# Optimization experiments

Hardware: AMD Instinct MI355X
Metric: run time of the kernel (lower is better)

Reference implementation:

```python
import jax, jax.numpy as jnp
import numpy as np

B, L, E, D, H, N_ENT = 64, 50, 50, 100, 100, 200000


def setup_inputs() -> dict:
    key = jax.random.key(0)
    ks = jax.random.split(key, 12)
    neighbor_ids = jax.random.randint(ks[0], (B, L, E), 0, N_ENT)
    # 0/1 adjacency; mimic GraphConstructer: symmetric with self-loops
    adj = jax.random.randint(ks[1], (B, L, E, E), 0, 2).astype(jnp.int32)
    adj = jnp.maximum(adj, adj.transpose(0, 1, 3, 2))
    adj = jnp.maximum(adj, jnp.eye(E, dtype=jnp.int32))
    s = 0.1  # ~ 1/sqrt(D) init scale
    emb = jax.random.normal(ks[2], (N_ENT, D), jnp.float32) * s
    Wq = jax.random.normal(ks[3], (D, H), jnp.float32) * s
    bq = jax.random.normal(ks[4], (H,), jnp.float32) * s
    Wk = jax.random.normal(ks[5], (D, H), jnp.float32) * s
    bk = jax.random.normal(ks[6], (H,), jnp.float32) * s
    Wv = jax.random.normal(ks[7], (D, H), jnp.float32) * s
    bv = jax.random.normal(ks[8], (H,), jnp.float32) * s
    Ws = jax.random.normal(ks[9], (D, H), jnp.float32) * s
    bs = jax.random.normal(ks[10], (H,), jnp.float32) * s
    return {"neighbor_ids": neighbor_ids, "adj": adj, "emb": emb,
            "Wq": Wq, "bq": bq, "Wk": Wk, "bk": bk,
            "Wv": Wv, "bv": bv, "Ws": Ws, "bs": bs}


def reference(neighbor_ids, adj, emb, Wq, bq, Wk, bk, Wv, bv, Ws, bs):
    b, l, e = neighbor_ids.shape
    d = emb.shape[1]
    h = Wq.shape[1]
    # embedding gather: [B,L,E,D] -> [G,E,D], G = B*L graphs
    x = emb[neighbor_ids].reshape(b * l, e, d)
    a = adj.reshape(b * l, e, e)
    # TransformerConv (heads=1): q,k,v linear with bias
    q = x @ Wq + bq
    k = x @ Wk + bk
    v = x @ Wv + bv
    scores = jnp.einsum('gid,gjd->gij', q, k) / jnp.sqrt(jnp.asarray(h, x.dtype))
    # edge (j -> i) exists when adj[j, i] != 0; target i attends over sources j
    mask = a.transpose(0, 2, 1) != 0  # mask[g, i, j]
    neg = jnp.finfo(scores.dtype).min
    attn = jax.nn.softmax(jnp.where(mask, scores, neg), axis=-1)
    # nodes with no incoming edge aggregate to zero (PyG softmax/scatter semantics)
    attn = jnp.where(mask.any(-1, keepdims=True), attn, jnp.zeros((), attn.dtype))
    agg = jnp.einsum('gij,gjd->gid', attn, v)
    out = agg + x @ Ws + bs  # root/skip connection with bias
    # take center node (index 0) of each ego-graph -> [B, L, H]
    return out.reshape(b, l, e, h)[:, :, 0, :]
```

## Files before the change

kernel.cpp:

```cpp
#include <hip/hip_runtime.h>
#include <math.h>

#define E_N 50
#define D_N 100
#define H_N 100
#define XSTR 51
#define GT 8
#define NTHR 256
#define GATHER_IT 5

__device__ __forceinline__ float bf2f(unsigned int s16) {
    return __uint_as_float(s16 << 16);
}

__device__ __forceinline__ unsigned short f2bf(float f) {
    unsigned int u = __float_as_uint(f);
    unsigned int r = (u + 0x7FFFu + ((u >> 16) & 1u)) >> 16;
    return (unsigned short)r;
}

template <bool F32>
__device__ __forceinline__ float ldx(const void* p, int i) {
    if (F32) return reinterpret_cast<const float*>(p)[i];
    return bf2f(reinterpret_cast<const unsigned short*>(p)[i]);
}

template <bool F32>
__device__ __forceinline__ float4 ld4(const void* p, long long i4) {
    if (F32) return reinterpret_cast<const float4*>(p)[i4];
    uint2 v = reinterpret_cast<const uint2*>(p)[i4];
    float4 f;
    f.x = bf2f(v.x & 0xFFFFu);
    f.y = bf2f(v.x >> 16);
    f.z = bf2f(v.y & 0xFFFFu);
    f.w = bf2f(v.y >> 16);
    return f;
}

__device__ __forceinline__ int sniff_f32(const void* emb, int tid, int* slot) {
    if (tid < 64) {
        unsigned short hw = reinterpret_cast<const unsigned short*>(emb)[tid * 2];
        float v = bf2f(hw);
        float a = fabsf(v);
        int sane = (v == 0.f) || (a >= 1e-4f && a <= 8.0f);
        unsigned long long ball = __ballot(sane);
        if (tid == 0) *slot = (__popcll(ball) < 32) ? 1 : 0;
    }
    __syncthreads();
    return *slot;
}

template <bool F32>
__device__ __forceinline__ void precomp_core(
    int dp, int tid, const void* __restrict__ Wq, const void* __restrict__ bq,
    const void* __restrict__ Wk, float* __restrict__ At, float* __restrict__ c,
    float* wq_s, float* bq_s)
{
    if (tid < H_N) wq_s[tid] = ldx<F32>(Wq, dp * H_N + tid);
    if (dp == 0 && tid < H_N) bq_s[tid] = ldx<F32>(bq, tid);
    __syncthreads();
    if (tid < D_N) {
        float a0 = 0.f, a1 = 0.f, a2 = 0.f, a3 = 0.f;
        #pragma unroll
        for (int h4 = 0; h4 < H_N / 4; ++h4) {
            float4 w = ld4<F32>(Wk, (long long)tid * (H_N / 4) + h4);
            a0 = fmaf(w.x, wq_s[h4 * 4 + 0], a0);
            a1 = fmaf(w.y, wq_s[h4 * 4 + 1], a1);
            a2 = fmaf(w.z, wq_s[h4 * 4 + 2], a2);
            a3 = fmaf(w.w, wq_s[h4 * 4 + 3], a3);
        }
        At[dp * D_N + tid] = (a0 + a1) + (a2 + a3);
        if (dp == 0) {
            float c0 = 0.f, c1 = 0.f, c2 = 0.f, c3 = 0.f;
            #pragma unroll
            for (int h4 = 0; h4 < H_N / 4; ++h4) {
                float4 w = ld4<F32>(Wk, (long long)tid * (H_N / 4) + h4);
                c0 = fmaf(w.x, bq_s[h4 * 4 + 0], c0);
                c1 = fmaf(w.y, bq_s[h4 * 4 + 1], c1);
                c2 = fmaf(w.z, bq_s[h4 * 4 + 2], c2);
                c3 = fmaf(w.w, bq_s[h4 * 4 + 3], c3);
            }
            c[tid] = (c0 + c1) + (c2 + c3);
        }
    }
}

__global__ __launch_bounds__(128)
void precomp_kernel(const void* __restrict__ Wq, const void* __restrict__ bq,
                    const void* __restrict__ Wk, const void* __restrict__ emb,
                    float* __restrict__ At, float* __restrict__ c)
{
    __shared__ float wq_s[H_N];
    __shared__ float bq_s[H_N];
    __shared__ int is_f32_s;
    int f32 = sniff_f32(emb, threadIdx.x, &is_f32_s);
    if (f32) precomp_core<true >(blockIdx.x, threadIdx.x, Wq, bq, Wk, At, c, wq_s, bq_s);
    else     precomp_core<false>(blockIdx.x, threadIdx.x, Wq, bq, Wk, At, c, wq_s, bq_s);
}

template <bool F32>
__device__ __forceinline__ void ka_core(
    int g0, int G, int tid,
    const int* __restrict__ nbr, const void* __restrict__ emb,
    const float* __restrict__ At, const float* __restrict__ c,
    const void* __restrict__ Ws,
    float* __restrict__ wl, float* __restrict__ skip, float* x0s)
{
    if (tid < GT * (D_N / 4)) {
        int q = tid / (D_N / 4), d4 = tid - q * (D_N / 4);
        int gq = g0 + q; if (gq >= G) gq = G - 1;
        int id0 = nbr[gq * E_N];
        float4 v = ld4<F32>(emb, (long long)id0 * (D_N / 4) + d4);
        reinterpret_cast<float4*>(x0s + q * D_N)[d4] = v;
    }
    __syncthreads();

    if (tid < D_N) {
        int d = tid;
        float cv = c[d];
        float acc[GT];
        #pragma unroll
        for (int q = 0; q < GT; ++q) acc[q] = cv;
        #pragma unroll 4
        for (int dp = 0; dp < D_N; ++dp) {
            float a = At[dp * D_N + d];
            #pragma unroll
            for (int q = 0; q < GT; ++q)
                acc[q] = fmaf(a, x0s[q * D_N + dp], acc[q]);
        }
        #pragma unroll
        for (int q = 0; q < GT; ++q) {
            int gq = g0 + q;
            if (gq < G) wl[(size_t)gq * D_N + d] = acc[q];
        }
    } else if (tid >= 128 && tid < 128 + H_N) {
        int h = tid - 128;
        float acc[GT];
        #pragma unroll
        for (int q = 0; q < GT; ++q) acc[q] = 0.f;
        #pragma unroll 4
        for (int d = 0; d < D_N; ++d) {
            float w = ldx<F32>(Ws, d * H_N + h);
            #pragma unroll
            for (int q = 0; q < GT; ++q)
                acc[q] = fmaf(w, x0s[q * D_N + d], acc[q]);
        }
        #pragma unroll
        for (int q = 0; q < GT; ++q) {
            int gq = g0 + q;
            if (gq < G) skip[(size_t)gq * H_N + h] = acc[q];
        }
    }
}

__global__ __launch_bounds__(NTHR)
void ka_kernel(const int* __restrict__ nbr, const void* __restrict__ emb,
               const float* __restrict__ At, const float* __restrict__ c,
               const void* __restrict__ Ws,
               float* __restrict__ wl, float* __restrict__ skip, int G)
{
    __shared__ __align__(16) float x0s[GT * D_N];
    __shared__ int is_f32_s;
    int f32 = sniff_f32(emb, threadIdx.x, &is_f32_s);
    if (f32) ka_core<true >(blockIdx.x * GT, G, threadIdx.x, nbr, emb, At, c, Ws, wl, skip, x0s);
    else     ka_core<false>(blockIdx.x * GT, G, threadIdx.x, nbr, emb, At, c, Ws, wl, skip, x0s);
}

template <bool F32>
__device__ __forceinline__ void kb_core(
    int g, int tid,
    const int* __restrict__ nbr, const int* __restrict__ adj,
    const void* __restrict__ emb,
    const float* __restrict__ wl, float* __restrict__ y, float* __restrict__ den,
    float* xs, float* wls, float* ps)
{
    float wlv = (tid < D_N) ? wl[(size_t)g * D_N + tid] : 0.f;
    int mk = (tid < E_N) ? adj[(size_t)g * (E_N * E_N) + tid * E_N] : 0;
    int idr[GATHER_IT];
    #pragma unroll
    for (int r = 0; r < GATHER_IT; ++r) {
        int i = tid + NTHR * r;
        idr[r] = (i < E_N * (D_N / 4)) ? nbr[g * E_N + i / 25] : 0;
    }
    if (tid < D_N) wls[tid] = wlv;

    #pragma unroll
    for (int r = 0; r < GATHER_IT; ++r) {
        int i = tid + NTHR * r;
        if (i < E_N * (D_N / 4)) {
            int j  = i / 25;
            int d4 = i - j * 25;
            float4 v = ld4<F32>(emb, (long long)idr[r] * (D_N / 4) + d4);
            int d0 = d4 * 4;
            xs[(d0 + 0) * XSTR + j] = v.x;
            xs[(d0 + 1) * XSTR + j] = v.y;
            xs[(d0 + 2) * XSTR + j] = v.z;
            xs[(d0 + 3) * XSTR + j] = v.w;
        }
    }
    __syncthreads();

    if (tid < 64) {
        float s = 0.f;
        if (tid < E_N) {
            #pragma unroll 10
            for (int d = 0; d < D_N; ++d)
                s = fmaf(wls[d], xs[d * XSTR + tid], s);
            s *= 0.1f;
        }
        bool live = (tid < E_N) && (mk != 0);
        float m = live ? s : -3.0e38f;
        #pragma unroll
        for (int off = 32; off; off >>= 1)
            m = fmaxf(m, __shfl_xor(m, off));
        float e = live ? __expf(s - m) : 0.f;
        float dn = e;
        #pragma unroll
        for (int off = 32; off; off >>= 1)
            dn += __shfl_xor(dn, off);
        float inv = dn > 0.f ? 1.0f / dn : 0.f;
        if (tid < E_N) ps[tid] = e * inv;
        if (tid == 0)  den[g] = dn;
    }
    __syncthreads();

    if (tid < D_N) {
        float acc = 0.f;
        #pragma unroll 10
        for (int j = 0; j < E_N; ++j)
            acc = fmaf(ps[j], xs[tid * XSTR + j], acc);
        y[(size_t)g * D_N + tid] = acc;
    }
}

__global__ __launch_bounds__(NTHR)
void kb_kernel(const int* __restrict__ nbr, const int* __restrict__ adj,
               const void* __restrict__ emb,
               const float* __restrict__ wl, float* __restrict__ y,
               float* __restrict__ den, int G)
{
    __shared__ __align__(16) float xs[D_N * XSTR];
    __shared__ __align__(16) float wls[D_N];
    __shared__ __align__(16) float ps[E_N];
    __shared__ int is_f32_s;
    int f32 = sniff_f32(emb, threadIdx.x, &is_f32_s);
    if (f32) kb_core<true >(blockIdx.x, threadIdx.x, nbr, adj, emb, wl, y, den, xs, wls, ps);
    else     kb_core<false>(blockIdx.x, threadIdx.x, nbr, adj, emb, wl, y, den, xs, wls, ps);
}

template <bool F32>
__device__ __forceinline__ void kc_core(
    int g0, int G, int tid,
    const void* __restrict__ Wv, const void* __restrict__ bv,
    const void* __restrict__ bs,
    const float* __restrict__ skip, const float* __restrict__ y,
    const float* __restrict__ den, void* __restrict__ out,
    float* ys, float* denf)
{
    if (tid < GT * (D_N / 4)) {
        int q = tid / (D_N / 4), d4 = tid - q * (D_N / 4);
        int gq = g0 + q; if (gq >= G) gq = G - 1;
        reinterpret_cast<float4*>(ys + q * D_N)[d4] =
            reinterpret_cast<const float4*>(y + (size_t)gq * D_N)[d4];
    }
    if (tid < GT) {
        int gq = g0 + tid; if (gq >= G) gq = G - 1;
        denf[tid] = den[gq];
    }
    __syncthreads();

    int half = tid >> 7;
    int hh = tid & 127;
    if (hh < H_N) {
        int h = hh, qb = half * 4;
        float b   = ldx<F32>(bs, h);
        float bvv = ldx<F32>(bv, h);
        float acc[4];
        #pragma unroll
        for (int q2 = 0; q2 < 4; ++q2) {
            int gq = g0 + qb + q2; if (gq >= G) gq = G - 1;
            acc[q2] = b + (denf[qb + q2] > 0.f ? bvv : 0.f) + skip[(size_t)gq * H_N + h];
        }
        #pragma unroll 4
        for (int d = 0; d < D_N; ++d) {
            float w = ldx<F32>(Wv, d * H_N + h);
            #pragma unroll
            for (int q2 = 0; q2 < 4; ++q2)
                acc[q2] = fmaf(w, ys[(qb + q2) * D_N + d], acc[q2]);
        }
        #pragma unroll
        for (int q2 = 0; q2 < 4; ++q2) {
            int gq = g0 + qb + q2;
            if (gq < G) {
                size_t o = (size_t)gq * H_N + h;
                if (F32) reinterpret_cast<float*>(out)[o] = acc[q2];
                else     reinterpret_cast<unsigned short*>(out)[o] = f2bf(acc[q2]);
            }
        }
    }
}

__global__ __launch_bounds__(NTHR)
void kc_kernel(const void* __restrict__ Wv, const void* __restrict__ bv,
               const void* __restrict__ bs, const void* __restrict__ emb,
               const float* __restrict__ skip, const float* __restrict__ y,
               const float* __restrict__ den, void* __restrict__ out, int G)
{
    __shared__ __align__(16) float ys[GT * D_N];
    __shared__ float denf[GT];
    __shared__ int is_f32_s;
    int f32 = sniff_f32(emb, threadIdx.x, &is_f32_s);
    if (f32) kc_core<true >(blockIdx.x * GT, G, threadIdx.x, Wv, bv, bs, skip, y, den, out, ys, denf);
    else     kc_core<false>(blockIdx.x * GT, G, threadIdx.x, Wv, bv, bs, skip, y, den, out, ys, denf);
}

extern "C" void kernel_launch(void* const* d_in, const int* in_sizes, int n_in,
                              void* d_out, int out_size, void* d_ws, size_t ws_size,
                              hipStream_t stream) {
    const int* nbr = (const int*)d_in[0];
    const int* adj = (const int*)d_in[1];
    const void* emb = d_in[2];
    const void* Wq  = d_in[3];
    const void* bq  = d_in[4];
    const void* Wk  = d_in[5];
    const void* Wv  = d_in[7];
    const void* bv  = d_in[8];
    const void* Ws  = d_in[9];
    const void* bs  = d_in[10];

    const int G = in_sizes[0] / E_N;

    float* At   = (float*)d_ws;
    float* c    = At + D_N * D_N;
    float* wl   = c + D_N;
    float* skip = wl + (size_t)G * D_N;
    float* y    = skip + (size_t)G * H_N;
    float* den  = y + (size_t)G * D_N;

    const int GB = (G + GT - 1) / GT;
    precomp_kernel<<<D_N, 128, 0, stream>>>(Wq, bq, Wk, emb, At, c);
    ka_kernel<<<GB, NTHR, 0, stream>>>(nbr, emb, At, c, Ws, wl, skip, G);
    kb_kernel<<<G, NTHR, 0, stream>>>(nbr, adj, emb, wl, y, den, G);
    kc_kernel<<<GB, NTHR, 0, stream>>>(Wv, bv, bs, emb, skip, y, den, d_out, G);
}
```

Before: 189.9 us.

## Fuse ka/kb/kc into one kernel processing two graphs per block with direct-to-LDS gathers

Replaces the three per-stage kernels (center projection, attention, output projection) with a single fused kernel in which each block handles two ego-graphs. Embedding rows are gathered straight into LDS with global_load_lds, and in the bf16 path they stay packed as bf16 pairs. Fusing removes the intermediate wl/skip/y/den round trips through global memory and two kernel launches. In exchange each block now reads the full Wv and Ws weights for only two graphs instead of amortising them over eight, and the adjacency mask load changes from a column to a row (valid because adj is symmetric).

```diff
diff --git a/kernel.cpp b/kernel.cpp
--- a/kernel.cpp
+++ b/kernel.cpp
@@ -4,25 +4,25 @@
 #define E_N 50
 #define D_N 100
 #define H_N 100
-#define XSTR 51
-#define GT 8
 #define NTHR 256
-#define GATHER_IT 5
-
-__device__ __forceinline__ float bf2f(unsigned int s16) {
-    return __uint_as_float(s16 << 16);
-}
-
-__device__ __forceinline__ unsigned short f2bf(float f) {
-    unsigned int u = __float_as_uint(f);
-    unsigned int r = (u + 0x7FFFu + ((u >> 16) & 1u)) >> 16;
-    return (unsigned short)r;
+#define GG (E_N * E_N)
+
+typedef unsigned int u32;
+typedef unsigned short u16;
+typedef __attribute__((address_space(1))) const void gvoid;
+typedef __attribute__((address_space(3))) void lvoid;
+
+__device__ __forceinline__ float bf2f(u32 s16) { return __uint_as_float(s16 << 16); }
+
+__device__ __forceinline__ u16 f2bf(float f) {
+    u32 u = __float_as_uint(f);
+    return (u16)((u + 0x7FFFu + ((u >> 16) & 1u)) >> 16);
 }
 
 template <bool F32>
 __device__ __forceinline__ float ldx(const void* p, int i) {
     if (F32) return reinterpret_cast<const float*>(p)[i];
-    return bf2f(reinterpret_cast<const unsigned short*>(p)[i]);
+    return bf2f(reinterpret_cast<const u16*>(p)[i]);
 }
 
 template <bool F32>
@@ -39,7 +39,7 @@
 
 __device__ __forceinline__ int sniff_f32(const void* emb, int tid, int* slot) {
     if (tid < 64) {
-        unsigned short hw = reinterpret_cast<const unsigned short*>(emb)[tid * 2];
+        u16 hw = reinterpret_cast<const u16*>(emb)[tid * 2];
         float v = bf2f(hw);
         float a = fabsf(v);
         int sane = (v == 0.f) || (a >= 1e-4f && a <= 8.0f);
@@ -98,105 +98,179 @@
     else     precomp_core<false>(blockIdx.x, threadIdx.x, Wq, bq, Wk, At, c, wq_s, bq_s);
 }
 
-template <bool F32>
-__device__ __forceinline__ void ka_core(
-    int g0, int G, int tid,
-    const int* __restrict__ nbr, const void* __restrict__ emb,
-    const float* __restrict__ At, const float* __restrict__ c,
-    const void* __restrict__ Ws,
-    float* __restrict__ wl, float* __restrict__ skip, float* x0s)
-{
-    if (tid < GT * (D_N / 4)) {
-        int q = tid / (D_N / 4), d4 = tid - q * (D_N / 4);
-        int gq = g0 + q; if (gq >= G) gq = G - 1;
-        int id0 = nbr[gq * E_N];
-        float4 v = ld4<F32>(emb, (long long)id0 * (D_N / 4) + d4);
-        reinterpret_cast<float4*>(x0s + q * D_N)[d4] = v;
-    }
-    __syncthreads();
-
-    if (tid < D_N) {
-        int d = tid;
-        float cv = c[d];
-        float acc[GT];
-        #pragma unroll
-        for (int q = 0; q < GT; ++q) acc[q] = cv;
-        #pragma unroll 4
-        for (int dp = 0; dp < D_N; ++dp) {
-            float a = At[dp * D_N + d];
-            #pragma unroll
-            for (int q = 0; q < GT; ++q)
-                acc[q] = fmaf(a, x0s[q * D_N + dp], acc[q]);
-        }
-        #pragma unroll
-        for (int q = 0; q < GT; ++q) {
-            int gq = g0 + q;
-            if (gq < G) wl[(size_t)gq * D_N + d] = acc[q];
-        }
-    } else if (tid >= 128 && tid < 128 + H_N) {
-        int h = tid - 128;
-        float acc[GT];
-        #pragma unroll
-        for (int q = 0; q < GT; ++q) acc[q] = 0.f;
-        #pragma unroll 4
-        for (int d = 0; d < D_N; ++d) {
-            float w = ldx<F32>(Ws, d * H_N + h);
-            #pragma unroll
-            for (int q = 0; q < GT; ++q)
-                acc[q] = fmaf(w, x0s[q * D_N + d], acc[q]);
-        }
-        #pragma unroll
-        for (int q = 0; q < GT; ++q) {
-            int gq = g0 + q;
-            if (gq < G) skip[(size_t)gq * H_N + h] = acc[q];
-        }
-    }
-}
-
-__global__ __launch_bounds__(NTHR)
-void ka_kernel(const int* __restrict__ nbr, const void* __restrict__ emb,
-               const float* __restrict__ At, const float* __restrict__ c,
-               const void* __restrict__ Ws,
-               float* __restrict__ wl, float* __restrict__ skip, int G)
-{
-    __shared__ __align__(16) float x0s[GT * D_N];
-    __shared__ int is_f32_s;
-    int f32 = sniff_f32(emb, threadIdx.x, &is_f32_s);
-    if (f32) ka_core<true >(blockIdx.x * GT, G, threadIdx.x, nbr, emb, At, c, Ws, wl, skip, x0s);
-    else     ka_core<false>(blockIdx.x * GT, G, threadIdx.x, nbr, emb, At, c, Ws, wl, skip, x0s);
-}
-
-template <bool F32>
-__device__ __forceinline__ void kb_core(
-    int g, int tid,
+__device__ __forceinline__ void core_bf16(
+    int g0, int g1, int G, int tid,
     const int* __restrict__ nbr, const int* __restrict__ adj,
     const void* __restrict__ emb,
-    const float* __restrict__ wl, float* __restrict__ y, float* __restrict__ den,
-    float* xs, float* wls, float* ps)
-{
-    float wlv = (tid < D_N) ? wl[(size_t)g * D_N + tid] : 0.f;
-    int mk = (tid < E_N) ? adj[(size_t)g * (E_N * E_N) + tid * E_N] : 0;
-    int idr[GATHER_IT];
-    #pragma unroll
-    for (int r = 0; r < GATHER_IT; ++r) {
-        int i = tid + NTHR * r;
-        idr[r] = (i < E_N * (D_N / 4)) ? nbr[g * E_N + i / 25] : 0;
-    }
-    if (tid < D_N) wls[tid] = wlv;
-
-    #pragma unroll
-    for (int r = 0; r < GATHER_IT; ++r) {
-        int i = tid + NTHR * r;
-        if (i < E_N * (D_N / 4)) {
-            int j  = i / 25;
-            int d4 = i - j * 25;
-            float4 v = ld4<F32>(emb, (long long)idr[r] * (D_N / 4) + d4);
-            int d0 = d4 * 4;
-            xs[(d0 + 0) * XSTR + j] = v.x;
-            xs[(d0 + 1) * XSTR + j] = v.y;
-            xs[(d0 + 2) * XSTR + j] = v.z;
-            xs[(d0 + 3) * XSTR + j] = v.w;
-        }
+    const float* __restrict__ At, const float* __restrict__ c,
+    const void* __restrict__ Wv, const void* __restrict__ bv,
+    const void* __restrict__ Ws, const void* __restrict__ bs,
+    void* __restrict__ out,
+    u32* xsu, float* wls, float* ps, float* ys, float* dens)
+{
+    int mk = 0;
+    {
+        int w = tid >> 6, j = tid & 63;
+        if (w < 2 && j < E_N)
+            mk = adj[(size_t)(w ? g1 : g0) * GG + j];
+    }
+
+    const u16* e16 = (const u16*)emb;
+    {
+        int idr[10];
+        #pragma unroll
+        for (int r = 0; r < 10; ++r) {
+            int i = tid + NTHR * r;
+            idr[r] = (i < GG) ? nbr[g0 * E_N + i / 50] : 0;
+        }
+        #pragma unroll
+        for (int r = 0; r < 10; ++r) {
+            int i = tid + NTHR * r;
+            if (i < GG) {
+                int j = i / 50, cc = i - j * 50;
+                const u16* ga = e16 + (size_t)idr[r] * D_N + cc * 2;
+                u32* lb = xsu + (NTHR * r + (tid & ~63));
+                __builtin_amdgcn_global_load_lds((gvoid*)ga, (lvoid*)lb, 4, 0, 0);
+            }
+        }
+    }
+    {
+        int idr[10];
+        #pragma unroll
+        for (int r = 0; r < 10; ++r) {
+            int i = tid + NTHR * r;
+            idr[r] = (i < GG) ? nbr[g1 * E_N + i / 50] : 0;
+        }
+        #pragma unroll
+        for (int r = 0; r < 10; ++r) {
+            int i = tid + NTHR * r;
+            if (i < GG) {
+                int j = i / 50, cc = i - j * 50;
+                const u16* ga = e16 + (size_t)idr[r] * D_N + cc * 2;
+                u32* lb = xsu + GG + (NTHR * r + (tid & ~63));
+                __builtin_amdgcn_global_load_lds((gvoid*)ga, (lvoid*)lb, 4, 0, 0);
+            }
+        }
+    }
+    __syncthreads();
+
+    if (tid < 2 * D_N) {
+        int q = tid / D_N, d = tid - q * D_N;
+        float acc = c[d];
+        const u32* x0 = xsu + q * GG;
+        #pragma unroll 4
+        for (int dp = 0; dp < D_N; dp += 2) {
+            u32 xp = x0[dp >> 1];
+            acc = fmaf(At[dp * D_N + d],       bf2f(xp & 0xFFFFu), acc);
+            acc = fmaf(At[(dp + 1) * D_N + d], bf2f(xp >> 16),     acc);
+        }
+        wls[q * D_N + d] = acc;
+    }
+    __syncthreads();
+
+    if (tid < 128) {
+        int w = tid >> 6, j = tid & 63;
+        float s = 0.f;
+        if (j < E_N) {
+            const u32* xr = xsu + w * GG + j * 50;
+            const float* wv = wls + w * D_N;
+            #pragma unroll 5
+            for (int d2 = 0; d2 < 50; ++d2) {
+                u32 xp = xr[d2];
+                s = fmaf(bf2f(xp & 0xFFFFu), wv[2 * d2],     s);
+                s = fmaf(bf2f(xp >> 16),     wv[2 * d2 + 1], s);
+            }
+            s *= 0.1f;
+        }
+        bool live = (j < E_N) && (mk != 0);
+        float m = live ? s : -3.0e38f;
+        #pragma unroll
+        for (int off = 32; off; off >>= 1)
+            m = fmaxf(m, __shfl_xor(m, off));
+        float e = live ? __expf(s - m) : 0.f;
+        float dn = e;
+        #pragma unroll
+        for (int off = 32; off; off >>= 1)
+            dn += __shfl_xor(dn, off);
+        float inv = dn > 0.f ? 1.0f / dn : 0.f;
+        if (j < E_N) ps[w * E_N + j] = e * inv;
+        if (j == 0)  dens[w] = dn;
+    }
+    __syncthreads();
+
+    if (tid < 2 * D_N) {
+        int q = tid / D_N, d = tid - q * D_N;
+        const u32* xq = xsu + q * GG + (d >> 1);
+        int hi = d & 1;
+        float acc = 0.f;
+        #pragma unroll 10
+        for (int j = 0; j < E_N; ++j) {
+            u32 xp = xq[j * 50];
+            acc = fmaf(ps[q * E_N + j], bf2f(hi ? (xp >> 16) : (xp & 0xFFFFu)), acc);
+        }
+        ys[q * D_N + d] = acc;
+    }
+    __syncthreads();
+
+    if (tid < 2 * H_N) {
+        int q = tid / H_N, h = tid - q * H_N;
+        float flag = dens[q] > 0.f ? 1.f : 0.f;
+        float acc = ldx<false>(bs, h) + ldx<false>(bv, h) * flag;
+        const u32* x0 = xsu + q * GG;
+        const float* yq = ys + q * D_N;
+        #pragma unroll 2
+        for (int dp = 0; dp < D_N; dp += 2) {
+            u32 xp = x0[dp >> 1];
+            acc = fmaf(yq[dp],     ldx<false>(Wv, dp * H_N + h),       acc);
+            acc = fmaf(yq[dp + 1], ldx<false>(Wv, (dp + 1) * H_N + h), acc);
+            acc = fmaf(bf2f(xp & 0xFFFFu), ldx<false>(Ws, dp * H_N + h),       acc);
+            acc = fmaf(bf2f(xp >> 16),     ldx<false>(Ws, (dp + 1) * H_N + h), acc);
+        }
+        if (g0 + q < G) {
+            size_t o = (size_t)(q ? g1 : g0) * H_N + h;
+            ((u16*)out)[o] = f2bf(acc);
+        }
+    }
+}
+
+__device__ __forceinline__ void core_f32_one(
+    int g, int valid, int tid,
+    const int* __restrict__ nbr, const int* __restrict__ adj,
+    const void* __restrict__ emb,
+    const float* __restrict__ At, const float* __restrict__ c,
+    const void* __restrict__ Wv, const void* __restrict__ bv,
+    const void* __restrict__ Ws, const void* __restrict__ bs,
+    void* __restrict__ out,
+    float* xs , float* wls, float* ps, float* ys, float* dens)
+{
+    int mk = (tid < E_N) ? adj[(size_t)g * GG + tid] : 0;
+    const float* ef = (const float*)emb;
+    {
+        int idr[5];
+        #pragma unroll
+        for (int r = 0; r < 5; ++r) {
+            int i = tid + NTHR * r;
+            idr[r] = (i < E_N * 25) ? nbr[g * E_N + i / 25] : 0;
+        }
+        #pragma unroll
+        for (int r = 0; r < 5; ++r) {
+            int i = tid + NTHR * r;
+            if (i < E_N * 25) {
+                int j = i / 25, d4 = i - j * 25;
+                const float* ga = ef + (size_t)idr[r] * D_N + d4 * 4;
+                float* lb = xs + 4 * (NTHR * r + (tid & ~63));
+                __builtin_amdgcn_global_load_lds((gvoid*)ga, (lvoid*)lb, 16, 0, 0);
+            }
+        }
+    }
+    __syncthreads();
+
+    if (tid < D_N) {
+        float acc = c[tid];
+        #pragma unroll 4
+        for (int dp = 0; dp < D_N; ++dp)
+            acc = fmaf(At[dp * D_N + tid], xs[dp], acc);
+        wls[tid] = acc;
     }
     __syncthreads();
 
@@ -205,7 +279,7 @@
         if (tid < E_N) {
             #pragma unroll 10
             for (int d = 0; d < D_N; ++d)
-                s = fmaf(wls[d], xs[d * XSTR + tid], s);
+                s = fmaf(wls[d], xs[tid * D_N + d], s);
             s *= 0.1f;
         }
         bool live = (tid < E_N) && (mk != 0);
@@ -220,7 +294,7 @@
             dn += __shfl_xor(dn, off);
         float inv = dn > 0.f ? 1.0f / dn : 0.f;
         if (tid < E_N) ps[tid] = e * inv;
-        if (tid == 0)  den[g] = dn;
+        if (tid == 0)  dens[0] = dn;
     }
     __syncthreads();
 
@@ -228,90 +302,54 @@
         float acc = 0.f;
         #pragma unroll 10
         for (int j = 0; j < E_N; ++j)
-            acc = fmaf(ps[j], xs[tid * XSTR + j], acc);
-        y[(size_t)g * D_N + tid] = acc;
-    }
-}
-
-__global__ __launch_bounds__(NTHR)
-void kb_kernel(const int* __restrict__ nbr, const int* __restrict__ adj,
-               const void* __restrict__ emb,
-               const float* __restrict__ wl, float* __restrict__ y,
-               float* __restrict__ den, int G)
-{
-    __shared__ __align__(16) float xs[D_N * XSTR];
-    __shared__ __align__(16) float wls[D_N];
-    __shared__ __align__(16) float ps[E_N];
-    __shared__ int is_f32_s;
-    int f32 = sniff_f32(emb, threadIdx.x, &is_f32_s);
-    if (f32) kb_core<true >(blockIdx.x, threadIdx.x, nbr, adj, emb, wl, y, den, xs, wls, ps);
-    else     kb_core<false>(blockIdx.x, threadIdx.x, nbr, adj, emb, wl, y, den, xs, wls, ps);
-}
-
-template <bool F32>
-__device__ __forceinline__ void kc_core(
-    int g0, int G, int tid,
-    const void* __restrict__ Wv, const void* __restrict__ bv,
-    const void* __restrict__ bs,
-    const float* __restrict__ skip, const float* __restrict__ y,
-    const float* __restrict__ den, void* __restrict__ out,
-    float* ys, float* denf)
-{
-    if (tid < GT * (D_N / 4)) {
-        int q = tid / (D_N / 4), d4 = tid - q * (D_N / 4);
-        int gq = g0 + q; if (gq >= G) gq = G - 1;
-        reinterpret_cast<float4*>(ys + q * D_N)[d4] =
-            reinterpret_cast<const float4*>(y + (size_t)gq * D_N)[d4];
-    }
-    if (tid < GT) {
-        int gq = g0 + tid; if (gq >= G) gq = G - 1;
-        denf[tid] = den[gq];
-    }
-    __syncthreads();
-
-    int half = tid >> 7;
-    int hh = tid & 127;
-    if (hh < H_N) {
-        int h = hh, qb = half * 4;
-        float b   = ldx<F32>(bs, h);
-        float bvv = ldx<F32>(bv, h);
-        float acc[4];
-        #pragma unroll
-        for (int q2 = 0; q2 < 4; ++q2) {
-            int gq = g0 + qb + q2; if (gq >= G) gq = G - 1;
-            acc[q2] = b + (denf[qb + q2] > 0.f ? bvv : 0.f) + skip[(size_t)gq * H_N + h];
-        }
+            acc = fmaf(ps[j], xs[j * D_N + tid], acc);
+        ys[tid] = acc;
+    }
+    __syncthreads();
+
+    if (tid < H_N && valid) {
+        float flag = dens[0] > 0.f ? 1.f : 0.f;
+        float acc = ldx<true>(bs, tid) + ldx<true>(bv, tid) * flag;
         #pragma unroll 4
         for (int d = 0; d < D_N; ++d) {
-            float w = ldx<F32>(Wv, d * H_N + h);
-            #pragma unroll
-            for (int q2 = 0; q2 < 4; ++q2)
-                acc[q2] = fmaf(w, ys[(qb + q2) * D_N + d], acc[q2]);
-        }
-        #pragma unroll
-        for (int q2 = 0; q2 < 4; ++q2) {
-            int gq = g0 + qb + q2;
-            if (gq < G) {
-                size_t o = (size_t)gq * H_N + h;
-                if (F32) reinterpret_cast<float*>(out)[o] = acc[q2];
-                else     reinterpret_cast<unsigned short*>(out)[o] = f2bf(acc[q2]);
-            }
-        }
-    }
-}
-
-__global__ __launch_bounds__(NTHR)
-void kc_kernel(const void* __restrict__ Wv, const void* __restrict__ bv,
-               const void* __restrict__ bs, const void* __restrict__ emb,
-               const float* __restrict__ skip, const float* __restrict__ y,
-               const float* __restrict__ den, void* __restrict__ out, int G)
-{
-    __shared__ __align__(16) float ys[GT * D_N];
-    __shared__ float denf[GT];
+            acc = fmaf(ys[d],  ldx<true>(Wv, d * H_N + tid), acc);
+            acc = fmaf(xs[d],  ldx<true>(Ws, d * H_N + tid), acc);
+        }
+        ((float*)out)[(size_t)g * H_N + tid] = acc;
+    }
+    __syncthreads();
+}
+
+__global__ __launch_bounds__(NTHR, 7)
+void fused2_kernel(const int* __restrict__ nbr, const int* __restrict__ adj,
+                   const void* __restrict__ emb,
+                   const float* __restrict__ At, const float* __restrict__ c,
+                   const void* __restrict__ Wv, const void* __restrict__ bv,
+                   const void* __restrict__ Ws, const void* __restrict__ bs,
+                   void* __restrict__ out, int G)
+{
+    __shared__ __align__(16) u32   xsu[2 * GG];
+    __shared__ __align__(16) float wls[2 * D_N];
+    __shared__ __align__(16) float ps [2 * E_N];
+    __shared__ __align__(16) float ys [2 * D_N];
+    __shared__ float dens[2];
     __shared__ int is_f32_s;
-    int f32 = sniff_f32(emb, threadIdx.x, &is_f32_s);
-    if (f32) kc_core<true >(blockIdx.x * GT, G, threadIdx.x, Wv, bv, bs, skip, y, den, out, ys, denf);
-    else     kc_core<false>(blockIdx.x * GT, G, threadIdx.x, Wv, bv, bs, skip, y, den, out, ys, denf);
+
+    int tid = threadIdx.x;
+    int g0 = blockIdx.x * 2;
+    int g1 = (g0 + 1 < G) ? g0 + 1 : G - 1;
+    int f32 = sniff_f32(emb, tid, &is_f32_s);
+
+    if (!f32) {
+        core_bf16(g0, g1, G, tid, nbr, adj, emb, At, c, Wv, bv, Ws, bs, out,
+                  xsu, wls, ps, ys, dens);
+    } else {
+        float* xsf = reinterpret_cast<float*>(xsu);
+        core_f32_one(g0, 1, tid, nbr, adj, emb, At, c, Wv, bv, Ws, bs, out,
+                     xsf, wls, ps, ys, dens);
+        core_f32_one(g1, g0 + 1 < G, tid, nbr, adj, emb, At, c, Wv, bv, Ws, bs, out,
+                     xsf, wls, ps, ys, dens);
+    }
 }
 
 extern "C" void kernel_launch(void* const* d_in, const int* in_sizes, int n_in,
@@ -330,16 +368,10 @@
 
     const int G = in_sizes[0] / E_N;
 
-    float* At   = (float*)d_ws;
-    float* c    = At + D_N * D_N;
-    float* wl   = c + D_N;
-    float* skip = wl + (size_t)G * D_N;
-    float* y    = skip + (size_t)G * H_N;
-    float* den  = y + (size_t)G * D_N;
-
-    const int GB = (G + GT - 1) / GT;
+    float* At = (float*)d_ws;
+    float* c  = At + D_N * D_N;
+
     precomp_kernel<<<D_N, 128, 0, stream>>>(Wq, bq, Wk, emb, At, c);
-    ka_kernel<<<GB, NTHR, 0, stream>>>(nbr, emb, At, c, Ws, wl, skip, G);
-    kb_kernel<<<G, NTHR, 0, stream>>>(nbr, adj, emb, wl, y, den, G);
-    kc_kernel<<<GB, NTHR, 0, stream>>>(Wv, bv, bs, emb, skip, y, den, d_out, G);
-}
+    fused2_kernel<<<(G + 1) / 2, NTHR, 0, stream>>>(nbr, adj, emb, At, c,
+                                                    Wv, bv, Ws, bs, d_out, G);
+}
```

Measured after the change: 185.9 us. 2.1% less time.
